# Optimization experiments

Measured on AMD Instinct MI355X. Metric: run time of the kernel, lower is better.

The kernel has to match this reference:

```python
import jax, jax.numpy as jnp
import numpy as np

DIM = 2048
B = 8192
RED = 16
FREQ = DIM // 2 + 1  # 1025


def setup_inputs() -> dict:
    key = jax.random.key(0)
    ks = jax.random.split(key, 8)
    s = 1.0 / np.sqrt(DIM)
    return {
        "x": jax.random.normal(ks[0], (B, DIM), dtype=jnp.float32),
        "W_in": jax.random.uniform(ks[1], (DIM, DIM), jnp.float32, -s, s),
        "b_in": jax.random.uniform(ks[2], (DIM,), jnp.float32, -s, s),
        "W_out": jax.random.uniform(ks[3], (DIM, DIM), jnp.float32, -s, s),
        "b_out": jax.random.uniform(ks[4], (DIM,), jnp.float32, -s, s),
        "freq_gate": jax.random.normal(ks[5], (FREQ, 2), dtype=jnp.float32) * 0.02,
        "W_fc1": jax.random.uniform(ks[6], (2 * DIM, DIM // RED), jnp.float32, -1.0 / np.sqrt(2 * DIM), 1.0 / np.sqrt(2 * DIM)),
        "W_fc2": jax.random.uniform(ks[7], (DIM // RED, DIM), jnp.float32, -1.0 / np.sqrt(DIM // RED), 1.0 / np.sqrt(DIM // RED)),
    }


def reference(x, W_in, b_in, W_out, b_out, freq_gate, W_fc1, W_fc2):
    # proj_in
    h = x @ W_in + b_in                      # [B, C]
    # FFT along feature dim, complex gating, inverse FFT
    hf = jnp.fft.rfft(h, axis=1)             # [B, C//2+1] complex
    gate = freq_gate[:, 0] + 1j * freq_gate[:, 1]
    hf = hf * gate[: hf.shape[1]]
    ht = jnp.fft.irfft(hf, n=h.shape[1], axis=1).astype(h.dtype)  # [B, C]
    # ChannelAttention on a 1x1 spatial map: both pools are identity
    # (original code uses AdaptiveAvgPool2d for BOTH avg and max branches)
    y = jnp.concatenate([ht, ht], axis=1)     # [B, 2C]
    y = jax.nn.relu(y @ W_fc1)                # [B, C//16]
    y = jax.nn.sigmoid(y @ W_fc2)             # [B, C]
    ht = ht * y
    # proj_out
    return ht @ W_out + b_out
```

## Files before the change

kernel.cpp:

```cpp
#include <hip/hip_runtime.h>

typedef unsigned short ushort_t;
typedef unsigned int uint_t;
typedef __attribute__((ext_vector_type(8))) short short8;
typedef __attribute__((ext_vector_type(4))) float f32x4;

#define DIM 2048
#define BATCH 8192

__device__ __forceinline__ ushort_t f2bf(float f) {
  union { float f; uint_t u; } x; x.f = f;
  uint_t r = x.u + 0x7fffu + ((x.u >> 16) & 1u);
  return (ushort_t)(r >> 16);
}
__device__ __forceinline__ float bf2f(ushort_t h) {
  union { uint_t u; float f; } x; x.u = ((uint_t)h) << 16; return x.f;
}

__device__ __forceinline__ void gload_lds16(const void* g, void* l) {
  typedef __attribute__((address_space(1))) const unsigned int gu32;
  typedef __attribute__((address_space(3))) unsigned int lu32;
  __builtin_amdgcn_global_load_lds((gu32*)g, (lu32*)l, 16, 0, 0);
}

__device__ __forceinline__ float block_reduce_sum(float v) {
  #pragma unroll
  for (int off = 32; off; off >>= 1) v += __shfl_down(v, off);
  __shared__ float red[4];
  int t = threadIdx.x;
  if ((t & 63) == 0) red[t >> 6] = v;
  __syncthreads();
  return red[0] + red[1] + red[2] + red[3];
}

__global__ void k_c(const float* __restrict__ fg, float* __restrict__ c) {
  int n = blockIdx.x;
  int t = threadIdx.x;
  float s = 0.f;
  for (int k = 1 + t; k < 1024; k += 256) {
    int r = (k * n) & 2047;
    float sn, cs;
    sincospif((float)r * (1.0f / 1024.0f), &sn, &cs);
    s += fg[2 * k] * cs - fg[2 * k + 1] * sn;
  }
  float tot = block_reduce_sum(s);
  if (t == 0) {
    float v = fg[0] + ((n & 1) ? -fg[2048] : fg[2048]) + 2.f * tot;
    c[n] = v * (1.0f / 2048.0f);
  }
}

__global__ void k_b1(const float* __restrict__ b_in, const float* __restrict__ c,
                     float* __restrict__ b1) {
  int n = blockIdx.x;
  int t = threadIdx.x;
  float s = 0.f;
  for (int m = t; m < 2048; m += 256) s += b_in[m] * c[(n - m) & 2047];
  float tot = block_reduce_sum(s);
  if (t == 0) b1[n] = tot;
}

__global__ void k_gt(const float* __restrict__ c, uint_t* __restrict__ gt) {
  int idx = blockIdx.x * 256 + threadIdx.x;
  int r = idx >> 10;
  int c2 = (idx & 1023) << 1;
  uint_t v0 = f2bf(c[(r - c2) & 2047]);
  uint_t v1 = f2bf(c[(r - c2 - 1) & 2047]);
  gt[idx] = v0 | (v1 << 16);
}

__global__ void k_cast4(const float* __restrict__ in, ushort_t* __restrict__ out) {
  long i = (long)blockIdx.x * 256 + threadIdx.x;
  float4 v = ((const float4*)in)[i];
  ushort4 o;
  o.x = f2bf(v.x); o.y = f2bf(v.y); o.z = f2bf(v.z); o.w = f2bf(v.w);
  ((ushort4*)out)[i] = o;
}

__global__ void k_tc(const float* __restrict__ in, ushort_t* __restrict__ out,
                     int R, int C) {
  __shared__ float tile[32][33];
  int bc = blockIdx.x * 32;
  int br = blockIdx.y * 32;
  int tx = threadIdx.x, ty = threadIdx.y;
  #pragma unroll
  for (int i = ty; i < 32; i += 8)
    tile[i][tx] = in[(size_t)(br + i) * C + bc + tx];
  __syncthreads();
  #pragma unroll
  for (int i = ty; i < 32; i += 8)
    out[(size_t)(bc + i) * R + br + tx] = f2bf(tile[tx][i]);
}

__global__ void k_fc1fold(const float* __restrict__ w, ushort_t* __restrict__ out) {
  int idx = blockIdx.x * 256 + threadIdx.x;
  int j = idx >> 11;
  int m = idx & 2047;
  out[idx] = f2bf(w[(size_t)m * 128 + j] + w[(size_t)(m + 2048) * 128 + j]);
}

__global__ void k_red4relu(const float* __restrict__ p, ushort_t* __restrict__ out) {
  int i = blockIdx.x * 256 + threadIdx.x;
  float s = p[i] + p[i + 1048576] + p[i + 2097152] + p[i + 3145728];
  out[i] = f2bf(s > 0.f ? s : 0.f);
}

template <int EPI>
__launch_bounds__(256, 2)
__global__ void gemm_bt(const ushort_t* __restrict__ A, const ushort_t* __restrict__ BT,
                        void* __restrict__ C, const float* __restrict__ bias,
                        const ushort_t* __restrict__ aux, int M, int N, int K) {
  __shared__ ushort_t ldsA[128 * 32];
  __shared__ ushort_t ldsB[128 * 32];
  const int t = threadIdx.x;
  const int wave = t >> 6, lane = t & 63;
  const int bm = blockIdx.x, bn = blockIdx.y;
  const int wr = wave >> 1, wc = wave & 1;
  const int lrow = lane & 15, lk = lane >> 4;

  f32x4 acc[4][4] = {};

  const size_t arow0 = (size_t)bm * 128;
  const size_t brow0 = (size_t)bn * 128;

  int kb = 0, ke = K;
  if constexpr (EPI == 5) { int ks = K >> 2; kb = blockIdx.z * ks; ke = kb + ks; }

  for (int k0 = kb; k0 < ke; k0 += 32) {
    if (k0 != kb) __syncthreads();
    #pragma unroll
    for (int h = 0; h < 2; ++h) {
      int q = t + h * 256;
      int row = q >> 2, slot = q & 3;
      int kc = slot ^ ((row >> 1) & 3);
      const ushort_t* ga = A + (arow0 + row) * K + k0 + kc * 8;
      gload_lds16(ga, &ldsA[(wave * 64 + h * 256) * 8]);
      const ushort_t* gb = BT + (brow0 + row) * K + k0 + kc * 8;
      gload_lds16(gb, &ldsB[(wave * 64 + h * 256) * 8]);
    }
    __syncthreads();

    short8 af[4], bfr[4];
    #pragma unroll
    for (int m = 0; m < 4; ++m) {
      int row = wr * 64 + m * 16 + lrow;
      int slot = lk ^ ((row >> 1) & 3);
      af[m] = *(const short8*)&ldsA[row * 32 + slot * 8];
      int rowb = wc * 64 + m * 16 + lrow;
      int slotb = lk ^ ((rowb >> 1) & 3);
      bfr[m] = *(const short8*)&ldsB[rowb * 32 + slotb * 8];
    }
    #pragma unroll
    for (int m = 0; m < 4; ++m)
      #pragma unroll
      for (int n = 0; n < 4; ++n)
        acc[m][n] = __builtin_amdgcn_mfma_f32_16x16x32_bf16(af[m], bfr[n], acc[m][n], 0, 0, 0);
  }

  const int rbase = bm * 128 + wr * 64;
  const int cbase = bn * 128 + wc * 64;
  #pragma unroll
  for (int m = 0; m < 4; ++m) {
    #pragma unroll
    for (int n = 0; n < 4; ++n) {
      int col = cbase + n * 16 + lrow;
      int row0 = rbase + m * 16 + lk * 4;
      #pragma unroll
      for (int j = 0; j < 4; ++j) {
        int r = row0 + j;
        float v = acc[m][n][j];
        size_t off = (size_t)r * N + col;
        if constexpr (EPI == 0) {
          ((ushort_t*)C)[off] = f2bf(v);
        } else if constexpr (EPI == 1) {
          ((ushort_t*)C)[off] = f2bf(v + bias[col]);
        } else if constexpr (EPI == 2) {
          ((ushort_t*)C)[off] = f2bf(v > 0.f ? v : 0.f);
        } else if constexpr (EPI == 3) {
          float y = 1.f / (1.f + __expf(-v));
          ((ushort_t*)C)[off] = f2bf(bf2f(aux[off]) * y);
        } else if constexpr (EPI == 4) {
          ((float*)C)[off] = v + bias[col];
        } else {
          ((float*)C)[off + (size_t)blockIdx.z * ((size_t)M * N)] = v;
        }
      }
    }
  }
}

__device__ __forceinline__ void stage_half(const ushort_t* __restrict__ src, size_t gr0,
                                           int k0b, int ksb, char* ldsHalf, int t) {
  #pragma unroll
  for (int l = 0; l < 2; ++l) {
    int p = (l * 512 + t) * 16;
    int row = p >> 7;
    int cb = (p & 127) ^ ((row & 7) << 4);
    const char* g = (const char*)src + (gr0 + row) * (size_t)ksb + k0b + cb;
    char* dst = ldsHalf + (l * 512 + (t & ~63)) * 16;
    gload_lds16(g, dst);
  }
}

__device__ __forceinline__ short8 ldfrag(const char* regionBase, int R, int kk, int lk) {
  int r = R & 127, h = R >> 7;
  int col = (kk * 64 + lk * 16) ^ ((r & 7) << 4);
  return *(const short8*)(regionBase + h * 16384 + r * 128 + col);
}

template <int EPI>
__launch_bounds__(512, 2)
__global__ void gemm256(const ushort_t* __restrict__ A, const ushort_t* __restrict__ BT,
                        void* __restrict__ C, const float* __restrict__ bias,
                        int N, int K, int nbn) {
  __shared__ __align__(16) char L[131072];
  const int t = threadIdx.x;
  const int lane = t & 63, wave = t >> 6;
  const int wm = wave >> 2, wn = wave & 3;
  const int lrow = lane & 15, lk = lane >> 4;

  int d = blockIdx.x;
  int cpx = gridDim.x >> 3;
  int wg = (d & 7) * cpx + (d >> 3);
  const int bm = wg / nbn, bn = wg % nbn;

  const size_t am0 = (size_t)bm * 256;
  const size_t bn0 = (size_t)bn * 256;
  const int ksb = K * 2;
  const int NT = K >> 6;

  f32x4 acc[8][4] = {};

  stage_half(A,  am0,       0,   ksb, L + 0,             t);
  stage_half(A,  am0 + 128, 0,   ksb, L + 16384,         t);
  stage_half(BT, bn0,       0,   ksb, L + 32768,         t);
  stage_half(BT, bn0 + 128, 0,   ksb, L + 49152,         t);
  stage_half(BT, bn0,       128, ksb, L + 65536 + 32768, t);
  stage_half(BT, bn0 + 128, 128, ksb, L + 65536 + 49152, t);
  asm volatile("s_waitcnt vmcnt(4)" ::: "memory");
  __builtin_amdgcn_s_barrier();

  short8 bfrag[4][2];
  short8 afrag[2][2];

  for (int T = 0; T < NT; T += 2) {
    int k1 = ((T + 1 < NT) ? T + 1 : NT - 1) * 128;
    int k2 = ((T + 2 < NT) ? T + 2 : NT - 1) * 128;
    int k3 = ((T + 3 < NT) ? T + 3 : NT - 1) * 128;
    #pragma unroll
    for (int ph = 0; ph < 8; ++ph) {
      const int cb = ph >> 2;
      const int cp = ph & 3;
      const char* Ab = L + cb * 65536;
      const char* Bb = L + cb * 65536 + 32768;
      if (cp == 0) {
        #pragma unroll
        for (int n = 0; n < 4; ++n)
          #pragma unroll
          for (int kk = 0; kk < 2; ++kk)
            bfrag[n][kk] = ldfrag(Bb, wn * 64 + n * 16 + lrow, kk, lk);
      }
      #pragma unroll
      for (int mi = 0; mi < 2; ++mi)
        #pragma unroll
        for (int kk = 0; kk < 2; ++kk)
          afrag[mi][kk] = ldfrag(Ab, wm * 128 + (cp * 2 + mi) * 16 + lrow, kk, lk);

      if (ph == 0) {
        stage_half(A, am0,       k1, ksb, L + 65536,         t);
        stage_half(A, am0 + 128, k1, ksb, L + 65536 + 16384, t);
      } else if (ph == 1) {
        stage_half(BT, bn0,       k2, ksb, L + 32768, t);
      } else if (ph == 2) {
        stage_half(BT, bn0 + 128, k2, ksb, L + 49152, t);
      } else if (ph == 3) {
        asm volatile("s_waitcnt vmcnt(4)" ::: "memory");
      } else if (ph == 4) {
        stage_half(A, am0,       k2, ksb, L + 0,     t);
      } else if (ph == 5) {
        stage_half(A, am0 + 128, k2, ksb, L + 16384, t);
      } else if (ph == 6) {
        stage_half(BT, bn0,       k3, ksb, L + 65536 + 32768, t);
      } else {
        stage_half(BT, bn0 + 128, k3, ksb, L + 65536 + 49152, t);
        asm volatile("s_waitcnt vmcnt(4)" ::: "memory");
      }

      __builtin_amdgcn_s_barrier();
      asm volatile("s_waitcnt lgkmcnt(0)" ::: "memory");
      __builtin_amdgcn_sched_barrier(0);
      __builtin_amdgcn_s_setprio(1);
      #pragma unroll
      for (int mi = 0; mi < 2; ++mi)
        #pragma unroll
        for (int n = 0; n < 4; ++n)
          #pragma unroll
          for (int kk = 0; kk < 2; ++kk)
            acc[cp * 2 + mi][n] = __builtin_amdgcn_mfma_f32_16x16x32_bf16(
                afrag[mi][kk], bfrag[n][kk], acc[cp * 2 + mi][n], 0, 0, 0);
      __builtin_amdgcn_s_setprio(0);
      __builtin_amdgcn_s_barrier();
    }
  }

  const int rbase = bm * 256 + wm * 128;
  const int cbase = bn * 256 + wn * 64;
  #pragma unroll
  for (int mi = 0; mi < 8; ++mi) {
    #pragma unroll
    for (int n = 0; n < 4; ++n) {
      int col = cbase + n * 16 + lrow;
      int row0 = rbase + mi * 16 + lk * 4;
      float bcol = bias[col];
      #pragma unroll
      for (int j = 0; j < 4; ++j) {
        float v = acc[mi][n][j] + bcol;
        size_t off = (size_t)(row0 + j) * N + col;
        if constexpr (EPI == 1) ((ushort_t*)C)[off] = f2bf(v);
        else                    ((float*)C)[off] = v;
      }
    }
  }
}

extern "C" void kernel_launch(void* const* d_in, const int* in_sizes, int n_in,
                              void* d_out, int out_size, void* d_ws, size_t ws_size,
                              hipStream_t stream) {
  const float* x     = (const float*)d_in[0];
  const float* W_in  = (const float*)d_in[1];
  const float* b_in  = (const float*)d_in[2];
  const float* W_out = (const float*)d_in[3];
  const float* b_out = (const float*)d_in[4];
  const float* fg    = (const float*)d_in[5];
  const float* W_fc1 = (const float*)d_in[6];
  const float* W_fc2 = (const float*)d_in[7];

  char* ws = (char*)d_ws;
  float*    c_buf  = (float*)(ws + 0);
  float*    b1     = (float*)(ws + 8192);
  ushort_t* WinBf  = (ushort_t*)(ws + 16384);
  ushort_t* W1T    = (ushort_t*)(ws + 8404992);
  ushort_t* WoutT  = (ushort_t*)(ws + 16793600);
  ushort_t* Wfc1eT = (ushort_t*)(ws + 25182208);
  ushort_t* Wfc2T  = (ushort_t*)(ws + 25706496);
  ushort_t* x_bf   = (ushort_t*)(ws + 26230784);
  float*    fcp    = (float*)(ws + 26230784);
  ushort_t* ht_bf  = (ushort_t*)(ws + 59785216);
  ushort_t* a_bf   = (ushort_t*)(ws + 93339648);
  ushort_t* GT     = (ushort_t*)(ws + 95436800);
  ushort_t* g_bf   = (ushort_t*)(ws + 95436800);
  (void)ws_size; (void)in_sizes; (void)n_in; (void)out_size;

  k_c<<<2048, 256, 0, stream>>>(fg, c_buf);
  k_b1<<<2048, 256, 0, stream>>>(b_in, c_buf, b1);
  k_gt<<<8192, 256, 0, stream>>>(c_buf, (uint_t*)GT);
  k_cast4<<<16384, 256, 0, stream>>>(x, x_bf);
  k_cast4<<<4096, 256, 0, stream>>>(W_in, WinBf);
  k_tc<<<dim3(64, 64), dim3(32, 8), 0, stream>>>(W_out, WoutT, 2048, 2048);
  k_tc<<<dim3(64, 4), dim3(32, 8), 0, stream>>>(W_fc2, Wfc2T, 128, 2048);
  k_fc1fold<<<1024, 256, 0, stream>>>(W_fc1, Wfc1eT);

  gemm_bt<0><<<dim3(16, 16), 256, 0, stream>>>(GT, WinBf, W1T, nullptr, nullptr,
                                               2048, 2048, 2048);
  gemm256<1><<<256, 512, 0, stream>>>(x_bf, W1T, ht_bf, b1, 2048, 2048, 8);
  gemm_bt<5><<<dim3(64, 1, 4), 256, 0, stream>>>(ht_bf, Wfc1eT, fcp, nullptr, nullptr,
                                                 8192, 128, 2048);
  k_red4relu<<<4096, 256, 0, stream>>>(fcp, a_bf);
  gemm_bt<3><<<dim3(64, 16), 256, 0, stream>>>(a_bf, Wfc2T, g_bf, nullptr, ht_bf,
                                               8192, 2048, 128);
  gemm256<4><<<256, 512, 0, stream>>>(g_bf, WoutT, (float*)d_out, b_out, 2048, 2048, 8);
}
```

Measured before the change: 377.0 us.

## Double-buffer LDS fragments in gemm256 and split-K the weight-fold GEMM

The main 256x256 GEMM now prefetches the next phase's A/B fragments from LDS into a second register set. It replaces the per-phase barrier plus full lgkmcnt(0) wait with partial lgkmcnt waits, and moves some vmcnt waits to earlier phases, so LDS reads overlap MFMA work. The 2048x2048 weight-fold GEMM (GT x W_in) is split four ways along K with fp32 partials and a reduce kernel, giving it 1024 workgroups instead of 256. This costs extra registers for the duplicated fragments, an extra partial-sum buffer and reduce pass, and relies on removing a barrier being safe for LDS reuse.

```diff
diff --git a/kernel.cpp b/kernel.cpp
--- a/kernel.cpp
+++ b/kernel.cpp
@@ -99,10 +99,12 @@
   out[idx] = f2bf(w[(size_t)m * 128 + j] + w[(size_t)(m + 2048) * 128 + j]);
 }
 
-__global__ void k_red4relu(const float* __restrict__ p, ushort_t* __restrict__ out) {
+template <int RELU>
+__global__ void k_red4(const float* __restrict__ p, ushort_t* __restrict__ out, int stride) {
   int i = blockIdx.x * 256 + threadIdx.x;
-  float s = p[i] + p[i + 1048576] + p[i + 2097152] + p[i + 3145728];
-  out[i] = f2bf(s > 0.f ? s : 0.f);
+  float s = p[i] + p[i + stride] + p[i + 2 * stride] + p[i + 3 * stride];
+  if constexpr (RELU) s = s > 0.f ? s : 0.f;
+  out[i] = f2bf(s);
 }
 
 template <int EPI>
@@ -240,8 +242,19 @@
   asm volatile("s_waitcnt vmcnt(4)" ::: "memory");
   __builtin_amdgcn_s_barrier();
 
-  short8 bfrag[4][2];
-  short8 afrag[2][2];
+  short8 bfr[2][4][2];
+  short8 afr[2][2][2];
+
+  #pragma unroll
+  for (int n = 0; n < 4; ++n)
+    #pragma unroll
+    for (int kk = 0; kk < 2; ++kk)
+      bfr[0][n][kk] = ldfrag(L + 32768, wn * 64 + n * 16 + lrow, kk, lk);
+  #pragma unroll
+  for (int mi = 0; mi < 2; ++mi)
+    #pragma unroll
+    for (int kk = 0; kk < 2; ++kk)
+      afr[0][mi][kk] = ldfrag(L + 0, wm * 128 + mi * 16 + lrow, kk, lk);
 
   for (int T = 0; T < NT; T += 2) {
     int k1 = ((T + 1 < NT) ? T + 1 : NT - 1) * 128;
@@ -251,20 +264,29 @@
     for (int ph = 0; ph < 8; ++ph) {
       const int cb = ph >> 2;
       const int cp = ph & 3;
-      const char* Ab = L + cb * 65536;
-      const char* Bb = L + cb * 65536 + 32768;
-      if (cp == 0) {
+      const int cur = ph & 1;
+
+      if (cp == 3) {
+        const char* ob = L + (cb ^ 1) * 65536;
         #pragma unroll
         for (int n = 0; n < 4; ++n)
           #pragma unroll
           for (int kk = 0; kk < 2; ++kk)
-            bfrag[n][kk] = ldfrag(Bb, wn * 64 + n * 16 + lrow, kk, lk);
+            bfr[cb ^ 1][n][kk] = ldfrag(ob + 32768, wn * 64 + n * 16 + lrow, kk, lk);
+        #pragma unroll
+        for (int mi = 0; mi < 2; ++mi)
+          #pragma unroll
+          for (int kk = 0; kk < 2; ++kk)
+            afr[cur ^ 1][mi][kk] = ldfrag(ob, wm * 128 + mi * 16 + lrow, kk, lk);
+      } else {
+        const char* Ab = L + cb * 65536;
+        #pragma unroll
+        for (int mi = 0; mi < 2; ++mi)
+          #pragma unroll
+          for (int kk = 0; kk < 2; ++kk)
+            afr[cur ^ 1][mi][kk] =
+                ldfrag(Ab, wm * 128 + ((cp + 1) * 2 + mi) * 16 + lrow, kk, lk);
       }
-      #pragma unroll
-      for (int mi = 0; mi < 2; ++mi)
-        #pragma unroll
-        for (int kk = 0; kk < 2; ++kk)
-          afrag[mi][kk] = ldfrag(Ab, wm * 128 + (cp * 2 + mi) * 16 + lrow, kk, lk);
 
       if (ph == 0) {
         stage_half(A, am0,       k1, ksb, L + 65536,         t);
@@ -273,7 +295,6 @@
         stage_half(BT, bn0,       k2, ksb, L + 32768, t);
       } else if (ph == 2) {
         stage_half(BT, bn0 + 128, k2, ksb, L + 49152, t);
-      } else if (ph == 3) {
         asm volatile("s_waitcnt vmcnt(4)" ::: "memory");
       } else if (ph == 4) {
         stage_half(A, am0,       k2, ksb, L + 0,     t);
@@ -281,13 +302,13 @@
         stage_half(A, am0 + 128, k2, ksb, L + 16384, t);
       } else if (ph == 6) {
         stage_half(BT, bn0,       k3, ksb, L + 65536 + 32768, t);
-      } else {
+        asm volatile("s_waitcnt vmcnt(2)" ::: "memory");
+      } else if (ph == 7) {
         stage_half(BT, bn0 + 128, k3, ksb, L + 65536 + 49152, t);
-        asm volatile("s_waitcnt vmcnt(4)" ::: "memory");
       }
 
-      __builtin_amdgcn_s_barrier();
-      asm volatile("s_waitcnt lgkmcnt(0)" ::: "memory");
+      if (cp == 3) asm volatile("s_waitcnt lgkmcnt(12)" ::: "memory");
+      else         asm volatile("s_waitcnt lgkmcnt(4)" ::: "memory");
       __builtin_amdgcn_sched_barrier(0);
       __builtin_amdgcn_s_setprio(1);
       #pragma unroll
@@ -297,7 +318,7 @@
           #pragma unroll
           for (int kk = 0; kk < 2; ++kk)
             acc[cp * 2 + mi][n] = __builtin_amdgcn_mfma_f32_16x16x32_bf16(
-                afrag[mi][kk], bfrag[n][kk], acc[cp * 2 + mi][n], 0, 0, 0);
+                afr[cur][mi][kk], bfr[cb][n][kk], acc[cp * 2 + mi][n], 0, 0, 0);
       __builtin_amdgcn_s_setprio(0);
       __builtin_amdgcn_s_barrier();
     }
@@ -311,13 +332,13 @@
     for (int n = 0; n < 4; ++n) {
       int col = cbase + n * 16 + lrow;
       int row0 = rbase + mi * 16 + lk * 4;
-      float bcol = bias[col];
+      float bcol = (EPI == 0) ? 0.f : bias[col];
       #pragma unroll
       for (int j = 0; j < 4; ++j) {
         float v = acc[mi][n][j] + bcol;
         size_t off = (size_t)(row0 + j) * N + col;
-        if constexpr (EPI == 1) ((ushort_t*)C)[off] = f2bf(v);
-        else                    ((float*)C)[off] = v;
+        if constexpr (EPI == 4) ((float*)C)[off] = v;
+        else                    ((ushort_t*)C)[off] = f2bf(v);
       }
     }
   }
@@ -343,6 +364,7 @@
   ushort_t* WoutT  = (ushort_t*)(ws + 16793600);
   ushort_t* Wfc1eT = (ushort_t*)(ws + 25182208);
   ushort_t* Wfc2T  = (ushort_t*)(ws + 25706496);
+  float*    foldp  = (float*)(ws + 26230784);
   ushort_t* x_bf   = (ushort_t*)(ws + 26230784);
   float*    fcp    = (float*)(ws + 26230784);
   ushort_t* ht_bf  = (ushort_t*)(ws + 59785216);
@@ -354,18 +376,21 @@
   k_c<<<2048, 256, 0, stream>>>(fg, c_buf);
   k_b1<<<2048, 256, 0, stream>>>(b_in, c_buf, b1);
   k_gt<<<8192, 256, 0, stream>>>(c_buf, (uint_t*)GT);
+  k_cast4<<<4096, 256, 0, stream>>>(W_in, WinBf);
+
+  gemm_bt<5><<<dim3(16, 16, 4), 256, 0, stream>>>(GT, WinBf, foldp, nullptr, nullptr,
+                                                  2048, 2048, 2048);
+  k_red4<0><<<16384, 256, 0, stream>>>(foldp, W1T, 4194304);
+
   k_cast4<<<16384, 256, 0, stream>>>(x, x_bf);
-  k_cast4<<<4096, 256, 0, stream>>>(W_in, WinBf);
   k_tc<<<dim3(64, 64), dim3(32, 8), 0, stream>>>(W_out, WoutT, 2048, 2048);
   k_tc<<<dim3(64, 4), dim3(32, 8), 0, stream>>>(W_fc2, Wfc2T, 128, 2048);
   k_fc1fold<<<1024, 256, 0, stream>>>(W_fc1, Wfc1eT);
 
-  gemm_bt<0><<<dim3(16, 16), 256, 0, stream>>>(GT, WinBf, W1T, nullptr, nullptr,
-                                               2048, 2048, 2048);
   gemm256<1><<<256, 512, 0, stream>>>(x_bf, W1T, ht_bf, b1, 2048, 2048, 8);
   gemm_bt<5><<<dim3(64, 1, 4), 256, 0, stream>>>(ht_bf, Wfc1eT, fcp, nullptr, nullptr,
                                                  8192, 128, 2048);
-  k_red4relu<<<4096, 256, 0, stream>>>(fcp, a_bf);
+  k_red4<1><<<4096, 256, 0, stream>>>(fcp, a_bf, 1048576);
   gemm_bt<3><<<dim3(64, 16), 256, 0, stream>>>(a_bf, Wfc2T, g_bf, nullptr, ht_bf,
                                                8192, 2048, 128);
   gemm256<4><<<256, 512, 0, stream>>>(g_bf, WoutT, (float*)d_out, b_out, 2048, 2048, 8);
```

After: 461.4 us. +22.4%, slower.
